# Kernel optimization log

Hardware: AMD Instinct MI355X
Metric: run time of the kernel (lower is better)

The kernel has to match this reference:

```python
import jax, jax.numpy as jnp
from jax import lax
import numpy as np

N_HEADS, N_FEATURES, IMG_W, IMG_H, C_DOWN = 8, 64, 96, 96, 32


def setup_inputs() -> dict:
    key = jax.random.key(0)
    ks = jax.random.split(key, 16)
    d = {
        'X': jax.random.normal(ks[0], (N_FEATURES, IMG_W, IMG_H), jnp.float32),
        'WQ_task': jax.random.normal(ks[1], (N_HEADS, N_FEATURES, 1, 1), jnp.float32),
        'BQ_task': jax.random.normal(ks[2], (N_HEADS, N_FEATURES, 1, 1), jnp.float32),
        'WK_task': jax.random.normal(ks[3], (N_FEATURES, 1, 1), jnp.float32),
        'BK_task': jax.random.normal(ks[4], (N_FEATURES, 1, 1), jnp.float32),
        'WV_task': jax.random.normal(ks[5], (1, C_DOWN, 1, 1), jnp.float32),
        'BV_task': jax.random.normal(ks[6], (1, C_DOWN, 1, 1), jnp.float32),
        # learned parameters (loaded from disk in the original)
        'WQ_t_minus_1': jax.random.uniform(ks[7], (N_HEADS, N_FEATURES, 1, 1), jnp.float32),
        'WQ_x': jax.random.uniform(ks[8], (1, N_FEATURES, 1, 1), jnp.float32),
        'BQ': jax.random.uniform(ks[9], (N_HEADS, N_FEATURES, 1, 1), jnp.float32),
        'WK_x': jax.random.uniform(ks[10], (N_FEATURES, 1, 1), jnp.float32),
        'BK': jax.random.uniform(ks[11], (N_FEATURES, 1, 1), jnp.float32),
        'Vconv_w': jax.random.normal(ks[12], (C_DOWN, N_FEATURES, 3, 3), jnp.float32) * 0.05,
        'Vconv_b': jax.random.normal(ks[13], (C_DOWN,), jnp.float32) * 0.05,
        # recurrent state (zeros at t=0 in original; random here to exercise the path)
        'prev_Q': jax.random.normal(ks[14], (N_HEADS, N_FEATURES, IMG_W, IMG_H), jnp.float32),
    }
    return d


def reference(X, WQ_task, BQ_task, WK_task, BK_task, WV_task, BV_task,
              WQ_t_minus_1, WQ_x, BQ, WK_x, BK, Vconv_w, Vconv_b, prev_Q):
    F, W, H = X.shape
    rx = X[None]  # (1, F, W, H)
    # Q: (A, F, W, H);  K: (F, W, H)
    Q = WQ_task * jax.nn.relu(WQ_t_minus_1 * prev_Q + WQ_x * rx + BQ) + BQ_task
    K = WK_task * jax.nn.relu(WK_x * X + BK) + BK_task
    # similarity[w,h,u,v] = sum_{a,f} Q[a,f,w,h] * K[f,u,v]
    #                     = sum_f (sum_a Q)[f,w,h] * K[f,u,v]  -> a (WH,F)@(F,WH) GEMM
    Qs = Q.sum(axis=0)  # (F, W, H)
    sim = jnp.einsum('fwh,fuv->whuv', Qs, K)  # (W, H, W, H)
    attn = jax.nn.softmax(sim.reshape(W, H, W * H), axis=-1)  # (W, H, WH)
    # V = task-modulated 3x3 conv of X
    Vc = lax.conv_general_dilated(rx, Vconv_w, window_strides=(1, 1), padding='SAME',
                                  dimension_numbers=('NCHW', 'OIHW', 'NCHW'))
    Vc = Vc + Vconv_b[None, :, None, None]
    V = (WV_task * Vc + BV_task)[0].reshape(C_DOWN, W * H)  # (C, WH)
    # out[c,w,h] = sum_k attn[w,h,k] * V[c,k]
    out = jnp.einsum('whk,ck->cwh', attn, V)  # (C, W, H)
    return out
```

## Files before the change

kernel.cpp:

```cpp
#include <hip/hip_runtime.h>

#define WH 9216
#define NF 64
#define NC 32
#define NH 8
#define IMGW 96
#define IMGH 96
#define PW 98
#define PPLANE 9604
#define L2E 1.4426950408889634f
#define DEFER 11.5f

typedef float f32x4 __attribute__((ext_vector_type(4)));
typedef short short8 __attribute__((ext_vector_type(8)));

__device__ inline short bf16_bits(float x) {
  __bf16 h = (__bf16)x;
  return __builtin_bit_cast(short, h);
}
__device__ inline float bf16_round(float x) { return (float)(__bf16)x; }

__global__ __launch_bounds__(256, 2) void pad_wpack_kernel(
    const float* __restrict__ X, const float* __restrict__ Wc,
    const float* __restrict__ WV_task,
    unsigned short* __restrict__ padXT, short8* __restrict__ wfrag)
{
  const int bid = blockIdx.x;
  const int t = threadIdx.x;
  if (bid < 301) {
    const int idx = bid * 256 + t;
    if (idx < 76832) {
      const int fi = idx / PPLANE;
      const int p = idx - fi * PPLANE;
      const int pw = p / PW;
      const int ph = p - pw * PW;
      short8 r;
      if (pw >= 1 && pw <= IMGW && ph >= 1 && ph <= IMGH) {
        const float* src = X + (size_t)fi * 8 * WH + (pw - 1) * IMGH + (ph - 1);
        #pragma unroll
        for (int e = 0; e < 8; ++e) r[e] = bf16_bits(src[(size_t)e * WH]);
      } else {
        #pragma unroll
        for (int e = 0; e < 8; ++e) r[e] = 0;
      }
      *(short8*)&padXT[(size_t)p * 64 + fi * 8] = r;
    }
  } else {
    #pragma unroll
    for (int j = 0; j < 9; ++j) {
      const int ridx = j * 256 + t;
      const int ct = ridx / 1152;
      const int rem = ridx - ct * 1152;
      const int cc = rem >> 6;
      const int lane = rem & 63;
      const int c = ct * 16 + (lane & 15);
      const int tap = cc >> 1;
      const int f0 = (cc & 1) * 32 + 8 * (lane >> 4);
      const float wv = WV_task[c];
      short8 r;
      #pragma unroll
      for (int e = 0; e < 8; ++e)
        r[e] = bf16_bits(wv * Wc[((size_t)c * NF + f0 + e) * 9 + tap]);
      wfrag[ridx] = r;
    }
  }
}

__global__ __launch_bounds__(256, 2) void qsk_vconv_kernel(
    const float* __restrict__ X, const float* __restrict__ WQ_task,
    const float* __restrict__ BQ_task, const float* __restrict__ WK_task,
    const float* __restrict__ BK_task, const float* __restrict__ WQ_t1,
    const float* __restrict__ WQ_x, const float* __restrict__ BQ,
    const float* __restrict__ WK_x, const float* __restrict__ BK,
    const float* __restrict__ prevQ,
    const unsigned short* __restrict__ padXT, const short8* __restrict__ wfrag,
    const float* __restrict__ bc, const float* __restrict__ WV_task,
    const float* __restrict__ BV_task,
    short* __restrict__ qfrag, short* __restrict__ kfrag,
    short* __restrict__ vfrag)
{
  __shared__ float Vt[2][32][20];
  const int bid = blockIdx.x;
  const int t = threadIdx.x;
  const int lane = t & 63;
  const int h = lane >> 4;
  if (bid < 576) {
    const int w2 = t >> 6;
    const int fh = w2 & 1, sub = w2 >> 1;
    const int T = bid;
    const int wh = T * 16 + (lane & 15);
    const int f0 = fh * 32 + 8 * h + 4 * sub;

    float x[4];
    #pragma unroll
    for (int e = 0; e < 4; ++e) x[e] = X[(size_t)(f0 + e) * WH + wh];
    float pq[32];
    #pragma unroll
    for (int a = 0; a < NH; ++a)
      #pragma unroll
      for (int e = 0; e < 4; ++e)
        pq[a * 4 + e] = prevQ[(size_t)(a * 64 + f0 + e) * WH + wh];

    const float4 wkx = *(const float4*)&WK_x[f0];
    const float4 bk  = *(const float4*)&BK[f0];
    const float4 wkt = *(const float4*)&WK_task[f0];
    const float4 bkt = *(const float4*)&BK_task[f0];
    const float4 wqx = *(const float4*)&WQ_x[f0];

    float q[4], k[4], xq[4];
    k[0] = fmaf(wkt.x, fmaxf(fmaf(wkx.x, x[0], bk.x), 0.f), bkt.x);
    k[1] = fmaf(wkt.y, fmaxf(fmaf(wkx.y, x[1], bk.y), 0.f), bkt.y);
    k[2] = fmaf(wkt.z, fmaxf(fmaf(wkx.z, x[2], bk.z), 0.f), bkt.z);
    k[3] = fmaf(wkt.w, fmaxf(fmaf(wkx.w, x[3], bk.w), 0.f), bkt.w);
    xq[0] = wqx.x * x[0]; xq[1] = wqx.y * x[1];
    xq[2] = wqx.z * x[2]; xq[3] = wqx.w * x[3];
    q[0] = q[1] = q[2] = q[3] = 0.f;
    #pragma unroll
    for (int a = 0; a < NH; ++a) {
      const int af0 = a * 64 + f0;
      const float4 w1  = *(const float4*)&WQ_t1[af0];
      const float4 bq  = *(const float4*)&BQ[af0];
      const float4 wqt = *(const float4*)&WQ_task[af0];
      const float4 bqt = *(const float4*)&BQ_task[af0];
      q[0] = fmaf(wqt.x, fmaxf(fmaf(w1.x, pq[a * 4 + 0], xq[0] + bq.x), 0.f), q[0]) + bqt.x;
      q[1] = fmaf(wqt.y, fmaxf(fmaf(w1.y, pq[a * 4 + 1], xq[1] + bq.y), 0.f), q[1]) + bqt.y;
      q[2] = fmaf(wqt.z, fmaxf(fmaf(w1.z, pq[a * 4 + 2], xq[2] + bq.z), 0.f), q[2]) + bqt.z;
      q[3] = fmaf(wqt.w, fmaxf(fmaf(w1.w, pq[a * 4 + 3], xq[3] + bq.w), 0.f), q[3]) + bqt.w;
    }

    short4 qh, ql, kh, klo;
    {
      float qs0 = q[0] * L2E, qs1 = q[1] * L2E, qs2 = q[2] * L2E, qs3 = q[3] * L2E;
      qh.x = bf16_bits(qs0); ql.x = bf16_bits(qs0 - bf16_round(qs0));
      qh.y = bf16_bits(qs1); ql.y = bf16_bits(qs1 - bf16_round(qs1));
      qh.z = bf16_bits(qs2); ql.z = bf16_bits(qs2 - bf16_round(qs2));
      qh.w = bf16_bits(qs3); ql.w = bf16_bits(qs3 - bf16_round(qs3));
      kh.x = bf16_bits(k[0]); klo.x = bf16_bits(k[0] - bf16_round(k[0]));
      kh.y = bf16_bits(k[1]); klo.y = bf16_bits(k[1] - bf16_round(k[1]));
      kh.z = bf16_bits(k[2]); klo.z = bf16_bits(k[2] - bf16_round(k[2]));
      kh.w = bf16_bits(k[3]); klo.w = bf16_bits(k[3] - bf16_round(k[3]));
    }
    const size_t offh = ((size_t)(T * 4 + fh) * 64 + lane) * 8 + sub * 4;
    const size_t offl = ((size_t)(T * 4 + 2 + fh) * 64 + lane) * 8 + sub * 4;
    *(short4*)&qfrag[offh] = qh;
    *(short4*)&qfrag[offl] = ql;
    *(short4*)&kfrag[offh] = kh;
    *(short4*)&kfrag[offl] = klo;
  } else {
    const int ktile = bid - 576;
    const int w = t >> 6;
    const int half = w & 1, ct = w >> 1;
    const int key = ktile * 16 + (lane & 15);
    const int kw = key / IMGH, kh = key - kw * IMGH;

    f32x4 acc = {0.f, 0.f, 0.f, 0.f};
    #pragma unroll
    for (int i = 0; i < 9; ++i) {
      const int cc = half * 9 + i;
      const int tap = cc >> 1;
      const int di = tap / 3, dj = tap - di * 3;
      const int f0 = (cc & 1) * 32 + 8 * h;
      const int sp = (kw + di) * PW + (kh + dj);
      const short8 xf = *(const short8*)&padXT[(size_t)sp * 64 + f0];
      acc = __builtin_amdgcn_mfma_f32_16x16x32_bf16(wfrag[(size_t)(ct * 18 + cc) * 64 + lane],
                                                    xf, acc, 0, 0, 0);
    }
    #pragma unroll
    for (int reg = 0; reg < 4; ++reg)
      Vt[half][ct * 16 + 4 * h + reg][lane & 15] = acc[reg];
    __syncthreads();
    if (t < 128) {
      const int ct2 = t >> 6;
      const int c = ct2 * 16 + (lane & 15);
      const float bias = fmaf(WV_task[c], bc[c], BV_task[c]);
      short4 r;
      #pragma unroll
      for (int j = 0; j < 4; ++j) {
        const int kl = 4 * h + j;
        r[j] = bf16_bits(Vt[0][c][kl] + Vt[1][c][kl] + bias);
      }
      const int chh = ktile >> 1, eh = ktile & 1;
      *(short4*)&vfrag[(((size_t)chh * 2 + ct2) * 64 + lane) * 8 + eh * 4] = r;
    }
  }
}

__global__ __launch_bounds__(256, 4) void flash_mfma(
    const short8* __restrict__ qfrag, const short8* __restrict__ kfrag,
    const short8* __restrict__ vfrag, float* __restrict__ part, int cps)
{
  const int t = threadIdx.x;
  const int lane = t & 63, wave = t >> 6;
  const int h = lane >> 4;
  const int qb = blockIdx.x;
  const int s = blockIdx.y;

  short8 qf[2][4];
  #pragma unroll
  for (int g = 0; g < 2; ++g)
    #pragma unroll
    for (int tm = 0; tm < 4; ++tm)
      qf[g][tm] = qfrag[((size_t)(qb * 2 + g) * 4 + tm) * 64 + lane];

  f32x4 acc[2][2];
  #pragma unroll
  for (int ct = 0; ct < 2; ++ct)
    #pragma unroll
    for (int g = 0; g < 2; ++g)
      acc[ct][g] = (f32x4){0.f, 0.f, 0.f, 0.f};
  float m[2] = {0.f, 0.f};
  float l[2] = {0.f, 0.f};

  const int cpw = cps >> 2;
  const int ch0 = s * cps + wave;
  #pragma unroll 2
  for (int it = 0; it < cpw; ++it) {
    const int ch = ch0 + it * 4;
    short8 kf[2][4];
    #pragma unroll
    for (int kt = 0; kt < 2; ++kt)
      #pragma unroll
      for (int tm = 0; tm < 4; ++tm)
        kf[kt][tm] = kfrag[((size_t)(2 * ch + kt) * 4 + tm) * 64 + lane];
    const short8 vf0 = vfrag[(size_t)(ch * 2 + 0) * 64 + lane];
    const short8 vf1 = vfrag[(size_t)(ch * 2 + 1) * 64 + lane];

    f32x4 st[2][2];
    __builtin_amdgcn_s_setprio(1);
    #pragma unroll
    for (int g = 0; g < 2; ++g) {
      const float nm = -m[g];
      f32x4 a0 = {nm, nm, nm, nm};
      f32x4 a1 = a0;
      a0 = __builtin_amdgcn_mfma_f32_16x16x32_bf16(kf[0][0], qf[g][0], a0, 0, 0, 0);
      a0 = __builtin_amdgcn_mfma_f32_16x16x32_bf16(kf[0][1], qf[g][1], a0, 0, 0, 0);
      a0 = __builtin_amdgcn_mfma_f32_16x16x32_bf16(kf[0][2], qf[g][0], a0, 0, 0, 0);
      a0 = __builtin_amdgcn_mfma_f32_16x16x32_bf16(kf[0][3], qf[g][1], a0, 0, 0, 0);
      a0 = __builtin_amdgcn_mfma_f32_16x16x32_bf16(kf[0][0], qf[g][2], a0, 0, 0, 0);
      a0 = __builtin_amdgcn_mfma_f32_16x16x32_bf16(kf[0][1], qf[g][3], a0, 0, 0, 0);
      a1 = __builtin_amdgcn_mfma_f32_16x16x32_bf16(kf[1][0], qf[g][0], a1, 0, 0, 0);
      a1 = __builtin_amdgcn_mfma_f32_16x16x32_bf16(kf[1][1], qf[g][1], a1, 0, 0, 0);
      a1 = __builtin_amdgcn_mfma_f32_16x16x32_bf16(kf[1][2], qf[g][0], a1, 0, 0, 0);
      a1 = __builtin_amdgcn_mfma_f32_16x16x32_bf16(kf[1][3], qf[g][1], a1, 0, 0, 0);
      a1 = __builtin_amdgcn_mfma_f32_16x16x32_bf16(kf[1][0], qf[g][2], a1, 0, 0, 0);
      a1 = __builtin_amdgcn_mfma_f32_16x16x32_bf16(kf[1][1], qf[g][3], a1, 0, 0, 0);
      st[g][0] = a0;
      st[g][1] = a1;
    }
    __builtin_amdgcn_s_setprio(0);

    short8 pb[2];
    #pragma unroll
    for (int g = 0; g < 2; ++g) {
      f32x4 st0 = st[g][0], st1 = st[g][1];
      const float loc = fmaxf(fmaxf(fmaxf(st0[0], st0[1]), fmaxf(st0[2], st0[3])),
                              fmaxf(fmaxf(st1[0], st1[1]), fmaxf(st1[2], st1[3])));
      if (__any(loc > DEFER)) {
        float tr = loc;
        tr = fmaxf(tr, __shfl_xor(tr, 16));
        tr = fmaxf(tr, __shfl_xor(tr, 32));
        const float d = fmaxf(tr, 0.f);
        const float r = exp2f(-d);
        l[g] *= r;
        acc[0][g] *= r;
        acc[1][g] *= r;
        m[g] += d;
        #pragma unroll
        for (int e = 0; e < 4; ++e) { st0[e] -= d; st1[e] -= d; }
      }
      float p0[4], p1[4];
      #pragma unroll
      for (int e = 0; e < 4; ++e) {
        p0[e] = exp2f(st0[e]);
        p1[e] = exp2f(st1[e]);
        pb[g][e] = bf16_bits(p0[e]);
        pb[g][4 + e] = bf16_bits(p1[e]);
      }
      l[g] += ((p0[0] + p0[1]) + (p0[2] + p0[3])) + ((p1[0] + p1[1]) + (p1[2] + p1[3]));
    }

    __builtin_amdgcn_s_setprio(1);
    #pragma unroll
    for (int g = 0; g < 2; ++g) {
      acc[0][g] = __builtin_amdgcn_mfma_f32_16x16x32_bf16(vf0, pb[g], acc[0][g], 0, 0, 0);
      acc[1][g] = __builtin_amdgcn_mfma_f32_16x16x32_bf16(vf1, pb[g], acc[1][g], 0, 0, 0);
    }
    __builtin_amdgcn_s_setprio(0);
  }

  const int u = s * 4 + wave;
  #pragma unroll
  for (int g = 0; g < 2; ++g) {
    float lf = l[g] + __shfl_xor(l[g], 16);
    lf += __shfl_xor(lf, 32);
    const int q = qb * 32 + g * 16 + (lane & 15);
    float* base = part + ((size_t)u * WH + q) * 36;
    *(f32x4*)(base + 0 + 4 * h) = acc[0][g];
    *(f32x4*)(base + 16 + 4 * h) = acc[1][g];
    if (h == 0) { base[32] = m[g]; base[33] = lf; }
  }
}

__global__ __launch_bounds__(256) void merge_kernel(
    const float* __restrict__ part, float* __restrict__ out, int units)
{
  const int t = threadIdx.x;
  const int cl = t & 31;
  const int wh = blockIdx.x * 8 + (t >> 5);
  float M = -1e30f, L = 0.f, A = 0.f;
  for (int u = 0; u < units; ++u) {
    const float* base = part + ((size_t)u * WH + wh) * 36;
    const float mu = base[32];
    const float lu = base[33];
    const float au = base[cl];
    if (mu > M) {
      const float sc = exp2f(M - mu);
      L = fmaf(L, sc, lu);
      A = fmaf(A, sc, au);
      M = mu;
    } else {
      const float e = exp2f(mu - M);
      L = fmaf(e, lu, L);
      A = fmaf(e, au, A);
    }
  }
  out[(size_t)cl * WH + wh] = A / L;
}

extern "C" void kernel_launch(void* const* d_in, const int* in_sizes, int n_in,
                              void* d_out, int out_size, void* d_ws, size_t ws_size,
                              hipStream_t stream)
{
  const float* X   = (const float*)d_in[0];
  const float* WQt = (const float*)d_in[1];
  const float* BQt = (const float*)d_in[2];
  const float* WKt = (const float*)d_in[3];
  const float* BKt = (const float*)d_in[4];
  const float* WVt = (const float*)d_in[5];
  const float* BVt = (const float*)d_in[6];
  const float* WQ1 = (const float*)d_in[7];
  const float* WQx = (const float*)d_in[8];
  const float* BQ  = (const float*)d_in[9];
  const float* WKx = (const float*)d_in[10];
  const float* BK  = (const float*)d_in[11];
  const float* Wc  = (const float*)d_in[12];
  const float* bc  = (const float*)d_in[13];
  const float* pQ  = (const float*)d_in[14];
  float* out = (float*)d_out;

  short8* qfrag = (short8*)d_ws;
  short8* kfrag = qfrag + (size_t)147456;
  short8* vfrag = kfrag + (size_t)147456;
  short8* wfrag = vfrag + (size_t)36864;
  unsigned short* padXT = (unsigned short*)(wfrag + 2304);
  float* part = (float*)((char*)padXT + (size_t)PPLANE * 64 * 2);
  const size_t base_bytes = ((size_t)147456 * 2 + 36864 + 2304) * 16 + (size_t)PPLANE * 64 * 2;

  int ksplit = 4;
  while (ksplit > 1 &&
         base_bytes + (size_t)(4 * ksplit) * WH * 36 * sizeof(float) > ws_size)
    ksplit >>= 1;
  const int cps = 288 / ksplit;
  const int units = 4 * ksplit;

  pad_wpack_kernel<<<dim3(302), 256, 0, stream>>>(X, Wc, WVt, padXT, wfrag);
  qsk_vconv_kernel<<<dim3(1152), 256, 0, stream>>>(X, WQt, BQt, WKt, BKt,
                                                   WQ1, WQx, BQ, WKx, BK, pQ,
                                                   padXT, wfrag, bc, WVt, BVt,
                                                   (short*)qfrag, (short*)kfrag,
                                                   (short*)vfrag);
  flash_mfma<<<dim3(288, ksplit), 256, 0, stream>>>(qfrag, kfrag, vfrag, part, cps);
  merge_kernel<<<dim3(WH / 8), 256, 0, stream>>>(part, out, units);
}
```

Measured before the change: 87.14 us.

## Share K/V chunks across waves via double-buffered LDS staging in flash kernel

The flash kernel is restructured so each wave owns one 16-query tile and all four waves of a block walk the same key chunks. Each chunk's K and V fragments are loaded cooperatively into a double-buffered LDS stage, with the next chunk prefetched while the current one is computed. Previously each wave loaded its own chunks from global memory. The row sum is now computed by an MFMA against a ones vector, bf16 packing uses v_cvt_pk_bf16_f32, and partial outputs go through nontemporal stores and loads. The split-K factor, grid shape and occupancy bound change to match, at the cost of a block-wide barrier on every iteration and one less wave group per SIMD.

Result: slower. 91.62 us (+5.1%).

```diff
diff --git a/kernel.cpp b/kernel.cpp
--- a/kernel.cpp
+++ b/kernel.cpp
@@ -13,12 +13,16 @@
 
 typedef float f32x4 __attribute__((ext_vector_type(4)));
 typedef short short8 __attribute__((ext_vector_type(8)));
+typedef int int4v __attribute__((ext_vector_type(4)));
 
 __device__ inline short bf16_bits(float x) {
   __bf16 h = (__bf16)x;
   return __builtin_bit_cast(short, h);
 }
 __device__ inline float bf16_round(float x) { return (float)(__bf16)x; }
+__device__ inline float fmax3(float a, float b, float c) {
+  return fmaxf(fmaxf(a, b), c);
+}
 
 __global__ __launch_bounds__(256, 2) void pad_wpack_kernel(
     const float* __restrict__ X, const float* __restrict__ Wc,
@@ -185,119 +189,140 @@
   }
 }
 
-__global__ __launch_bounds__(256, 4) void flash_mfma(
+__global__ __launch_bounds__(256, 3) void flash_mfma(
     const short8* __restrict__ qfrag, const short8* __restrict__ kfrag,
     const short8* __restrict__ vfrag, float* __restrict__ part, int cps)
 {
+  __shared__ short8 stage[2][12][64];
   const int t = threadIdx.x;
   const int lane = t & 63, wave = t >> 6;
   const int h = lane >> 4;
   const int qb = blockIdx.x;
   const int s = blockIdx.y;
-
-  short8 qf[2][4];
+  const int tile = qb * 4 + wave;
+
+  short8 qf[4];
   #pragma unroll
-  for (int g = 0; g < 2; ++g)
-    #pragma unroll
-    for (int tm = 0; tm < 4; ++tm)
-      qf[g][tm] = qfrag[((size_t)(qb * 2 + g) * 4 + tm) * 64 + lane];
-
-  f32x4 acc[2][2];
+  for (int tm = 0; tm < 4; ++tm)
+    qf[tm] = qfrag[((size_t)tile * 4 + tm) * 64 + lane];
+
+  short8 onesA = {0, 0, 0, 0, 0, 0, 0, 0};
+  if ((lane & 15) == 0) {
+    const short ob = bf16_bits(1.0f);
+    #pragma unroll
+    for (int e = 0; e < 8; ++e) onesA[e] = ob;
+  }
+
+  f32x4 acc0 = {0.f, 0.f, 0.f, 0.f};
+  f32x4 acc1 = {0.f, 0.f, 0.f, 0.f};
+  f32x4 acc2 = {0.f, 0.f, 0.f, 0.f};
+  float m = 0.f;
+
+  const int ch0 = s * cps;
   #pragma unroll
-  for (int ct = 0; ct < 2; ++ct)
-    #pragma unroll
-    for (int g = 0; g < 2; ++g)
-      acc[ct][g] = (f32x4){0.f, 0.f, 0.f, 0.f};
-  float m[2] = {0.f, 0.f};
-  float l[2] = {0.f, 0.f};
-
-  const int cpw = cps >> 2;
-  const int ch0 = s * cps + wave;
-  #pragma unroll 2
-  for (int it = 0; it < cpw; ++it) {
-    const int ch = ch0 + it * 4;
-    short8 kf[2][4];
-    #pragma unroll
-    for (int kt = 0; kt < 2; ++kt)
+  for (int i = 0; i < 3; ++i) {
+    const int r = wave + 4 * i;
+    const short8 v = (r < 8)
+        ? kfrag[((size_t)ch0 * 8 + r) * 64 + lane]
+        : ((r < 10) ? vfrag[((size_t)ch0 * 2 + (r - 8)) * 64 + lane]
+                    : kfrag[(size_t)ch0 * 8 * 64 + lane]);
+    stage[0][r][lane] = v;
+  }
+  __syncthreads();
+
+  int buf = 0;
+  for (int it = 0; it < cps; ++it) {
+    short8 tmp0, tmp1, tmp2;
+    const bool pre = (it + 1 < cps);
+    if (pre) {
+      const int ch = ch0 + it + 1;
+      const int r0 = wave, r1 = wave + 4, r2 = wave + 8;
+      tmp0 = kfrag[((size_t)ch * 8 + r0) * 64 + lane];
+      tmp1 = kfrag[((size_t)ch * 8 + r1) * 64 + lane];
+      tmp2 = (r2 < 10) ? vfrag[((size_t)ch * 2 + (r2 - 8)) * 64 + lane]
+                       : kfrag[(size_t)ch * 8 * 64 + lane];
+    }
+
+    short8 kf[8];
+    #pragma unroll
+    for (int r = 0; r < 8; ++r) kf[r] = stage[buf][r][lane];
+    const short8 vf0 = stage[buf][8][lane];
+    const short8 vf1 = stage[buf][9][lane];
+
+    const float nm = -m;
+    f32x4 a0 = {nm, nm, nm, nm};
+    f32x4 a1 = a0;
+    __builtin_amdgcn_s_setprio(1);
+    a0 = __builtin_amdgcn_mfma_f32_16x16x32_bf16(kf[0], qf[0], a0, 0, 0, 0);
+    a0 = __builtin_amdgcn_mfma_f32_16x16x32_bf16(kf[1], qf[1], a0, 0, 0, 0);
+    a0 = __builtin_amdgcn_mfma_f32_16x16x32_bf16(kf[2], qf[0], a0, 0, 0, 0);
+    a0 = __builtin_amdgcn_mfma_f32_16x16x32_bf16(kf[3], qf[1], a0, 0, 0, 0);
+    a0 = __builtin_amdgcn_mfma_f32_16x16x32_bf16(kf[0], qf[2], a0, 0, 0, 0);
+    a0 = __builtin_amdgcn_mfma_f32_16x16x32_bf16(kf[1], qf[3], a0, 0, 0, 0);
+    a1 = __builtin_amdgcn_mfma_f32_16x16x32_bf16(kf[4], qf[0], a1, 0, 0, 0);
+    a1 = __builtin_amdgcn_mfma_f32_16x16x32_bf16(kf[5], qf[1], a1, 0, 0, 0);
+    a1 = __builtin_amdgcn_mfma_f32_16x16x32_bf16(kf[6], qf[0], a1, 0, 0, 0);
+    a1 = __builtin_amdgcn_mfma_f32_16x16x32_bf16(kf[7], qf[1], a1, 0, 0, 0);
+    a1 = __builtin_amdgcn_mfma_f32_16x16x32_bf16(kf[4], qf[2], a1, 0, 0, 0);
+    a1 = __builtin_amdgcn_mfma_f32_16x16x32_bf16(kf[5], qf[3], a1, 0, 0, 0);
+    __builtin_amdgcn_s_setprio(0);
+
+    float loc = fmax3(a0[0], a0[1], a0[2]);
+    loc = fmax3(loc, a0[3], a1[0]);
+    loc = fmax3(loc, a1[1], a1[2]);
+    loc = fmaxf(loc, a1[3]);
+    if (__any(loc > DEFER)) {
+      float tr = loc;
+      tr = fmaxf(tr, __shfl_xor(tr, 16));
+      tr = fmaxf(tr, __shfl_xor(tr, 32));
+      const float d = fmaxf(tr, 0.f);
+      const float r = exp2f(-d);
+      acc0 *= r;
+      acc1 *= r;
+      acc2 *= r;
+      m += d;
       #pragma unroll
-      for (int tm = 0; tm < 4; ++tm)
-        kf[kt][tm] = kfrag[((size_t)(2 * ch + kt) * 4 + tm) * 64 + lane];
-    const short8 vf0 = vfrag[(size_t)(ch * 2 + 0) * 64 + lane];
-    const short8 vf1 = vfrag[(size_t)(ch * 2 + 1) * 64 + lane];
-
-    f32x4 st[2][2];
+      for (int e = 0; e < 4; ++e) { a0[e] -= d; a1[e] -= d; }
+    }
+    float p[8];
+    #pragma unroll
+    for (int e = 0; e < 4; ++e) {
+      p[e] = exp2f(a0[e]);
+      p[4 + e] = exp2f(a1[e]);
+    }
+    int w0, w1, w2, w3;
+    asm("v_cvt_pk_bf16_f32 %0, %1, %2" : "=v"(w0) : "v"(p[0]), "v"(p[1]));
+    asm("v_cvt_pk_bf16_f32 %0, %1, %2" : "=v"(w1) : "v"(p[2]), "v"(p[3]));
+    asm("v_cvt_pk_bf16_f32 %0, %1, %2" : "=v"(w2) : "v"(p[4]), "v"(p[5]));
+    asm("v_cvt_pk_bf16_f32 %0, %1, %2" : "=v"(w3) : "v"(p[6]), "v"(p[7]));
+    const int4v wi = {w0, w1, w2, w3};
+    const short8 pb = __builtin_bit_cast(short8, wi);
+
     __builtin_amdgcn_s_setprio(1);
-    #pragma unroll
-    for (int g = 0; g < 2; ++g) {
-      const float nm = -m[g];
-      f32x4 a0 = {nm, nm, nm, nm};
-      f32x4 a1 = a0;
-      a0 = __builtin_amdgcn_mfma_f32_16x16x32_bf16(kf[0][0], qf[g][0], a0, 0, 0, 0);
-      a0 = __builtin_amdgcn_mfma_f32_16x16x32_bf16(kf[0][1], qf[g][1], a0, 0, 0, 0);
-      a0 = __builtin_amdgcn_mfma_f32_16x16x32_bf16(kf[0][2], qf[g][0], a0, 0, 0, 0);
-      a0 = __builtin_amdgcn_mfma_f32_16x16x32_bf16(kf[0][3], qf[g][1], a0, 0, 0, 0);
-      a0 = __builtin_amdgcn_mfma_f32_16x16x32_bf16(kf[0][0], qf[g][2], a0, 0, 0, 0);
-      a0 = __builtin_amdgcn_mfma_f32_16x16x32_bf16(kf[0][1], qf[g][3], a0, 0, 0, 0);
-      a1 = __builtin_amdgcn_mfma_f32_16x16x32_bf16(kf[1][0], qf[g][0], a1, 0, 0, 0);
-      a1 = __builtin_amdgcn_mfma_f32_16x16x32_bf16(kf[1][1], qf[g][1], a1, 0, 0, 0);
-      a1 = __builtin_amdgcn_mfma_f32_16x16x32_bf16(kf[1][2], qf[g][0], a1, 0, 0, 0);
-      a1 = __builtin_amdgcn_mfma_f32_16x16x32_bf16(kf[1][3], qf[g][1], a1, 0, 0, 0);
-      a1 = __builtin_amdgcn_mfma_f32_16x16x32_bf16(kf[1][0], qf[g][2], a1, 0, 0, 0);
-      a1 = __builtin_amdgcn_mfma_f32_16x16x32_bf16(kf[1][1], qf[g][3], a1, 0, 0, 0);
-      st[g][0] = a0;
-      st[g][1] = a1;
-    }
+    acc0 = __builtin_amdgcn_mfma_f32_16x16x32_bf16(vf0, pb, acc0, 0, 0, 0);
+    acc1 = __builtin_amdgcn_mfma_f32_16x16x32_bf16(vf1, pb, acc1, 0, 0, 0);
+    acc2 = __builtin_amdgcn_mfma_f32_16x16x32_bf16(onesA, pb, acc2, 0, 0, 0);
     __builtin_amdgcn_s_setprio(0);
 
-    short8 pb[2];
-    #pragma unroll
-    for (int g = 0; g < 2; ++g) {
-      f32x4 st0 = st[g][0], st1 = st[g][1];
-      const float loc = fmaxf(fmaxf(fmaxf(st0[0], st0[1]), fmaxf(st0[2], st0[3])),
-                              fmaxf(fmaxf(st1[0], st1[1]), fmaxf(st1[2], st1[3])));
-      if (__any(loc > DEFER)) {
-        float tr = loc;
-        tr = fmaxf(tr, __shfl_xor(tr, 16));
-        tr = fmaxf(tr, __shfl_xor(tr, 32));
-        const float d = fmaxf(tr, 0.f);
-        const float r = exp2f(-d);
-        l[g] *= r;
-        acc[0][g] *= r;
-        acc[1][g] *= r;
-        m[g] += d;
-        #pragma unroll
-        for (int e = 0; e < 4; ++e) { st0[e] -= d; st1[e] -= d; }
-      }
-      float p0[4], p1[4];
-      #pragma unroll
-      for (int e = 0; e < 4; ++e) {
-        p0[e] = exp2f(st0[e]);
-        p1[e] = exp2f(st1[e]);
-        pb[g][e] = bf16_bits(p0[e]);
-        pb[g][4 + e] = bf16_bits(p1[e]);
-      }
-      l[g] += ((p0[0] + p0[1]) + (p0[2] + p0[3])) + ((p1[0] + p1[1]) + (p1[2] + p1[3]));
-    }
-
-    __builtin_amdgcn_s_setprio(1);
-    #pragma unroll
-    for (int g = 0; g < 2; ++g) {
-      acc[0][g] = __builtin_amdgcn_mfma_f32_16x16x32_bf16(vf0, pb[g], acc[0][g], 0, 0, 0);
-      acc[1][g] = __builtin_amdgcn_mfma_f32_16x16x32_bf16(vf1, pb[g], acc[1][g], 0, 0, 0);
-    }
-    __builtin_amdgcn_s_setprio(0);
-  }
-
-  const int u = s * 4 + wave;
+    if (pre) {
+      const int nb = buf ^ 1;
+      stage[nb][wave][lane] = tmp0;
+      stage[nb][wave + 4][lane] = tmp1;
+      stage[nb][wave + 8][lane] = tmp2;
+    }
+    __syncthreads();
+    buf ^= 1;
+  }
+
+  float* base = part + ((size_t)s * WH + tile * 16 + (lane & 15)) * 36;
   #pragma unroll
-  for (int g = 0; g < 2; ++g) {
-    float lf = l[g] + __shfl_xor(l[g], 16);
-    lf += __shfl_xor(lf, 32);
-    const int q = qb * 32 + g * 16 + (lane & 15);
-    float* base = part + ((size_t)u * WH + q) * 36;
-    *(f32x4*)(base + 0 + 4 * h) = acc[0][g];
-    *(f32x4*)(base + 16 + 4 * h) = acc[1][g];
-    if (h == 0) { base[32] = m[g]; base[33] = lf; }
+  for (int e = 0; e < 4; ++e) {
+    __builtin_nontemporal_store(acc0[e], base + 4 * h + e);
+    __builtin_nontemporal_store(acc1[e], base + 16 + 4 * h + e);
+  }
+  if (h == 0) {
+    __builtin_nontemporal_store(m, base + 32);
+    __builtin_nontemporal_store(acc2[0], base + 33);
   }
 }
 
@@ -310,9 +335,9 @@
   float M = -1e30f, L = 0.f, A = 0.f;
   for (int u = 0; u < units; ++u) {
     const float* base = part + ((size_t)u * WH + wh) * 36;
-    const float mu = base[32];
-    const float lu = base[33];
-    const float au = base[cl];
+    const float mu = __builtin_nontemporal_load(base + 32);
+    const float lu = __builtin_nontemporal_load(base + 33);
+    const float au = __builtin_nontemporal_load(base + cl);
     if (mu > M) {
       const float sc = exp2f(M - mu);
       L = fmaf(L, sc, lu);
@@ -356,12 +381,12 @@
   float* part = (float*)((char*)padXT + (size_t)PPLANE * 64 * 2);
   const size_t base_bytes = ((size_t)147456 * 2 + 36864 + 2304) * 16 + (size_t)PPLANE * 64 * 2;
 
-  int ksplit = 4;
+  int ksplit = 8;
   while (ksplit > 1 &&
-         base_bytes + (size_t)(4 * ksplit) * WH * 36 * sizeof(float) > ws_size)
+         base_bytes + (size_t)ksplit * WH * 36 * sizeof(float) > ws_size)
     ksplit >>= 1;
   const int cps = 288 / ksplit;
-  const int units = 4 * ksplit;
+  const int units = ksplit;
 
   pad_wpack_kernel<<<dim3(302), 256, 0, stream>>>(X, Wc, WVt, padXT, wfrag);
   qsk_vconv_kernel<<<dim3(1152), 256, 0, stream>>>(X, WQt, BQt, WKt, BKt,
@@ -369,6 +394,6 @@
                                                    padXT, wfrag, bc, WVt, BVt,
                                                    (short*)qfrag, (short*)kfrag,
                                                    (short*)vfrag);
-  flash_mfma<<<dim3(288, ksplit), 256, 0, stream>>>(qfrag, kfrag, vfrag, part, cps);
+  flash_mfma<<<dim3(144, ksplit), 256, 0, stream>>>(qfrag, kfrag, vfrag, part, cps);
   merge_kernel<<<dim3(WH / 8), 256, 0, stream>>>(part, out, units);
 }
```
